# Optimization experiments

Hardware: AMD Instinct MI355X
Metric: run time of the kernel (lower is better)

Reference implementation:

```python
import jax, jax.numpy as jnp
import numpy as np

# Dims derived from module build() with d_model=256
D_MODEL = 256
EXPAND = 2
D_STATE = 16
K_CONV = 4
CHUNK = 64
HEADDIM = 64
D_INNER = EXPAND * D_MODEL            # 512
NHEADS = D_INNER // HEADDIM           # 8
CONV_DIM = D_INNER + 2 * D_STATE      # 544
D_IN_PROJ = 3 * D_INNER + 2 * D_STATE + NHEADS  # 1576
BATCH, SEQ = 4, 4096


def setup_inputs() -> dict:
    key = jax.random.key(0)
    ks = jax.random.split(key, 11)
    def rn(k, shape, s=1.0):
        return jax.random.normal(k, shape, dtype=jnp.float32) * s
    return {
        "x": rn(ks[0], (BATCH, SEQ, D_MODEL)),
        "W_in": rn(ks[1], (D_MODEL, D_IN_PROJ), D_MODEL ** -0.5),
        "conv_w": rn(ks[2], (K_CONV, CONV_DIM), 0.3),
        "conv_b": rn(ks[3], (CONV_DIM,), 0.1),
        "A_log": rn(ks[4], (NHEADS, 2), 0.5),
        "dt_bias": rn(ks[5], (NHEADS,), 0.1),
        "D": rn(ks[6], (2 * NHEADS, 1), 0.5),
        "init_conv_state": rn(ks[7], (1, K_CONV, CONV_DIM), 0.1),
        "init_ssm_state": rn(ks[8], (1, 1, NHEADS, HEADDIM, D_STATE, 2), 0.1),
        "norm_w": rn(ks[9], (2 * D_INNER,), 0.5),
        "W_out": rn(ks[10], (2 * D_INNER, D_MODEL), (2 * D_INNER) ** -0.5),
    }


def _exp_segsum(a):
    # a: (..., T) complex. Returns exp(segsum(a)): lower-triangular (incl. diag)
    # with entry [i,j] = exp(sum_{j<d<=i} a_d), zero strictly above the diagonal.
    T = a.shape[-1]
    cs = jnp.cumsum(a, axis=-1)
    seg = cs[..., :, None] - cs[..., None, :]
    mask = jnp.tril(jnp.ones((T, T), dtype=bool))
    seg = jnp.where(mask, seg, 0.0)  # keep exp finite / grad-safe off-band
    return jnp.where(mask, jnp.exp(seg), 0.0)


def reference(x, W_in, conv_w, conv_b, A_log, dt_bias, D, init_conv_state,
              init_ssm_state, norm_w, W_out):
    b, L, _ = x.shape
    zxbcdt = x @ W_in  # (b, L, 3*d_inner + 2*d_state + nheads)
    z = zxbcdt[..., : 2 * D_INNER]
    xBC = zxbcdt[..., 2 * D_INNER: 3 * D_INNER + 2 * D_STATE]
    dt_raw = zxbcdt[..., 3 * D_INNER + 2 * D_STATE:]
    # dt scalar in call is 1/30, then *30 -> net factor 1
    dt = jnp.clip(jnp.exp(dt_raw + dt_bias), 0.0, 6.0)  # (b, L, h)

    # causal depthwise conv1d with learned initial conv state, relu6 activation
    prefix = jnp.broadcast_to(init_conv_state, (b, K_CONV, CONV_DIM))
    full = jnp.concatenate([prefix, xBC], axis=1)  # (b, K_CONV + L, conv_dim)
    conv = conv_b + sum(conv_w[j] * full[:, 1 + j: 1 + j + L] for j in range(K_CONV))
    xBC = jnp.clip(conv, 0.0, 6.0)  # relu6, last L of the L+1 valid outputs

    xin = xBC[..., :D_INNER]
    Bm = xBC[..., D_INNER: D_INNER + D_STATE].astype(jnp.complex64)
    Cm = xBC[..., D_INNER + D_STATE:].astype(jnp.complex64)
    xh = xin.reshape(b, L, NHEADS, HEADDIM).astype(jnp.complex64)

    A = -jnp.exp(A_log[:, 0]) + 1j * A_log[:, 1]  # (h,) complex
    dtc = dt.astype(jnp.complex64)
    Adt = A * dtc              # (b, L, h)
    xdt = xh * dtc[..., None]  # (b, L, h, p)

    # ---- chunked SSD (Mamba2-style) with complex state ----
    c = L // CHUNK
    xc = xdt.reshape(b, c, CHUNK, NHEADS, HEADDIM)
    Ac = Adt.reshape(b, c, CHUNK, NHEADS).transpose(0, 3, 1, 2)  # (b, h, c, l)
    Bc = Bm.reshape(b, c, CHUNK, D_STATE)
    Cc = Cm.reshape(b, c, CHUNK, D_STATE)

    A_cum = jnp.cumsum(Ac, axis=-1)          # (b, h, c, l)
    Lmat = _exp_segsum(Ac)                   # (b, h, c, l, l)
    Y_diag = jnp.einsum('bcln,bcsn,bhcls,bcshp->bclhp', Cc, Bc, Lmat, xc)

    decay_states = jnp.exp(A_cum[..., -1:] - A_cum)  # (b, h, c, l)
    states = jnp.einsum('bcln,bhcl,bclhp->bchpn', Bc, decay_states, xc)

    init_stat = init_ssm_state[:, 0, ..., 0] + 1j * init_ssm_state[:, 0, ..., 1]
    init_stat = jnp.broadcast_to(init_stat, (b, NHEADS, HEADDIM, D_STATE))[:, None]
    states = jnp.concatenate([init_stat, states], axis=1)  # (b, c+1, h, p, n)

    decay_chunk = _exp_segsum(jnp.pad(A_cum[..., -1], ((0, 0), (0, 0), (1, 0))))
    new_states = jnp.einsum('bhzc,bchpn->bzhpn', decay_chunk, states)
    Y_off = jnp.einsum('bcln,bchpn,bhcl->bclhp', Cc, new_states[:, :-1], jnp.exp(A_cum))

    Y = (Y_diag + Y_off).reshape(b, L, NHEADS, HEADDIM)  # complex

    # 'b l h p c -> b l (h c) p' : interleave real/imag per head
    y2 = jnp.stack([Y.real, Y.imag], axis=3).reshape(b, L, 2 * NHEADS, HEADDIM)
    xr = xin.reshape(b, L, NHEADS, HEADDIM)
    x2 = jnp.stack([xr, jnp.zeros_like(xr)], axis=3).reshape(b, L, 2 * NHEADS, HEADDIM)
    y2 = y2 + x2 * D  # D: (2h, 1) broadcasts over p
    y3 = y2.reshape(b, L, 2 * D_INNER)

    # RMSNorm gated by relu6(z)
    yz = y3 * jnp.clip(z, 0.0, 6.0)
    y4 = yz * jax.lax.rsqrt(jnp.mean(yz * yz, axis=-1, keepdims=True) + 1e-5) * norm_w
    return y4 @ W_out
```

## Files before the change

### kernel.cpp

```cpp
#include <hip/hip_runtime.h>
#include <math.h>

#define BATCHN 4
#define SEQL   4096
#define DMODEL 256
#define DIP    1576
#define DINNER 512
#define DZCOLS 1024
#define CONVD  544
#define NHEADS 8
#define HDIM   64
#define DSTATE 16
#define CHK    64
#define NCHUNK 64
#define MROWS  (BATCHN*SEQL)
#define NPAD   1664

typedef _Float16 half8 __attribute__((ext_vector_type(8)));
typedef _Float16 half4 __attribute__((ext_vector_type(4)));
typedef short    s16x8 __attribute__((ext_vector_type(8)));
typedef float    f32x4 __attribute__((ext_vector_type(4)));

__device__ __forceinline__ float clip6f(float x) { return fminf(fmaxf(x, 0.0f), 6.0f); }

__global__ __launch_bounds__(256) void k_cvt_x(const float* __restrict__ X,
                                               _Float16* __restrict__ A)
{
    const int gid = blockIdx.x * 256 + threadIdx.x;
    const float4 a = *reinterpret_cast<const float4*>(X + (size_t)gid * 8);
    const float4 b = *reinterpret_cast<const float4*>(X + (size_t)gid * 8 + 4);
    half8 h;
    h[0] = (_Float16)a.x; h[1] = (_Float16)a.y; h[2] = (_Float16)a.z; h[3] = (_Float16)a.w;
    h[4] = (_Float16)b.x; h[5] = (_Float16)b.y; h[6] = (_Float16)b.z; h[7] = (_Float16)b.w;
    *reinterpret_cast<half8*>(A + (size_t)gid * 8) = h;
}

__global__ __launch_bounds__(256) void k_cvt_win(const float* __restrict__ W,
                                                 _Float16* __restrict__ Bt)
{
    const int gid = blockIdx.x * 256 + threadIdx.x;
    const int k = gid & 255, n = gid >> 8;
    const float v = (n < DIP) ? W[(size_t)k * DIP + n] : 0.0f;
    Bt[gid] = (_Float16)v;
}

__global__ __launch_bounds__(256) void k_cvt_wout(const float* __restrict__ W,
                                                  const float* __restrict__ nw,
                                                  _Float16* __restrict__ Bt)
{
    const int gid = blockIdx.x * 256 + threadIdx.x;
    const int k = gid & 1023, n = gid >> 10;
    Bt[gid] = (_Float16)(W[(size_t)k * DMODEL + n] * nw[k]);
}

__global__ __launch_bounds__(256) void k_gemm_in(const _Float16* __restrict__ A,
                                                 const _Float16* __restrict__ Bt,
                                                 _Float16* __restrict__ zx,
                                                 float* __restrict__ dtraw)
{
    __shared__ _Float16 As[128 * 64];
    __shared__ _Float16 Bs[128 * 64];
    const int t  = threadIdx.x;
    const int orig = blockIdx.x;
    const int nid  = (orig & 7) * (13 * (MROWS / 128) / 8) + (orig >> 3);
    const int m0 = (nid / 13) * 128;
    const int n0 = (nid % 13) * 128;
    const int lane = t & 63, wid = t >> 6;
    const int wr = wid >> 1, wc = wid & 1;
    const int fr = lane & 15, fq = lane >> 4;
    const int lrow = lane >> 3;
    const int lch  = (lane & 7) ^ lrow;

    f32x4 acc[4][4];
#pragma unroll
    for (int m = 0; m < 4; ++m)
#pragma unroll
        for (int n = 0; n < 4; ++n)
#pragma unroll
            for (int e = 0; e < 4; ++e) acc[m][n][e] = 0.0f;

    for (int kt = 0; kt < DMODEL; kt += 64) {
#pragma unroll
        for (int q = 0; q < 4; ++q) {
            const int rbase = q * 32 + wid * 8;
            const size_t offA = (size_t)(m0 + rbase + lrow) * DMODEL + kt + lch * 8;
            const size_t offB = (size_t)(n0 + rbase + lrow) * DMODEL + kt + lch * 8;
            __builtin_amdgcn_global_load_lds(
                (const __attribute__((address_space(1))) void*)(A + offA),
                (__attribute__((address_space(3))) void*)(&As[rbase * 64]), 16, 0, 0);
            __builtin_amdgcn_global_load_lds(
                (const __attribute__((address_space(1))) void*)(Bt + offB),
                (__attribute__((address_space(3))) void*)(&Bs[rbase * 64]), 16, 0, 0);
        }
        __syncthreads();
#pragma unroll
        for (int ks = 0; ks < 64; ks += 32) {
            const int kc = (ks >> 3) + fq;
            half8 af[4], bf[4];
#pragma unroll
            for (int m = 0; m < 4; ++m) {
                const int R = wr * 64 + m * 16 + fr;
                af[m] = *reinterpret_cast<const half8*>(&As[R * 64 + ((kc ^ (R & 7)) << 3)]);
            }
#pragma unroll
            for (int n = 0; n < 4; ++n) {
                const int R = wc * 64 + n * 16 + fr;
                bf[n] = *reinterpret_cast<const half8*>(&Bs[R * 64 + ((kc ^ (R & 7)) << 3)]);
            }
#pragma unroll
            for (int m = 0; m < 4; ++m)
#pragma unroll
                for (int n = 0; n < 4; ++n)
                    acc[m][n] = __builtin_amdgcn_mfma_f32_16x16x32_f16(af[m], bf[n], acc[m][n], 0, 0, 0);
        }
        __syncthreads();
    }

#pragma unroll
    for (int m = 0; m < 4; ++m)
#pragma unroll
        for (int j = 0; j < 4; ++j) {
            const int row = m0 + wr * 64 + m * 16 + fq * 4 + j;
#pragma unroll
            for (int n = 0; n < 4; ++n) {
                const int col = n0 + wc * 64 + n * 16 + fr;
                const float v = acc[m][n][j];
                if (col < DIP) {
                    zx[(size_t)row * DIP + col] = (_Float16)v;
                    if (col >= 3 * DINNER + 2 * DSTATE)
                        dtraw[(size_t)row * 8 + (col - (3 * DINNER + 2 * DSTATE))] = v;
                }
            }
        }
}

__global__ __launch_bounds__(256) void k_conv(const _Float16* __restrict__ zx,
                                              const float* __restrict__ conv_w,
                                              const float* __restrict__ conv_b,
                                              const float* __restrict__ init_conv,
                                              _Float16* __restrict__ convout)
{
    const int NC8 = CONVD / 8;
    const int gid = blockIdx.x * 256 + threadIdx.x;
    if (gid >= MROWS * NC8) return;
    const int row  = gid / NC8;
    const int c    = (gid % NC8) * 8;
    const int b    = row / SEQL;
    const int tpos = row % SEQL;
    float acc[8];
    {
        const float4 b0 = *reinterpret_cast<const float4*>(conv_b + c);
        const float4 b1 = *reinterpret_cast<const float4*>(conv_b + c + 4);
        acc[0] = b0.x; acc[1] = b0.y; acc[2] = b0.z; acc[3] = b0.w;
        acc[4] = b1.x; acc[5] = b1.y; acc[6] = b1.z; acc[7] = b1.w;
    }
#pragma unroll
    for (int j = 0; j < 4; ++j) {
        const int srct = tpos - 3 + j;
        float v[8];
        if (srct >= 0) {
            const half8 hv = *reinterpret_cast<const half8*>(
                zx + (size_t)(b * SEQL + srct) * DIP + DZCOLS + c);
#pragma unroll
            for (int e = 0; e < 8; ++e) v[e] = (float)hv[e];
        } else {
            const float* ip = init_conv + (size_t)(tpos + 1 + j) * CONVD + c;
            const float4 i0 = *reinterpret_cast<const float4*>(ip);
            const float4 i1 = *reinterpret_cast<const float4*>(ip + 4);
            v[0] = i0.x; v[1] = i0.y; v[2] = i0.z; v[3] = i0.w;
            v[4] = i1.x; v[5] = i1.y; v[6] = i1.z; v[7] = i1.w;
        }
        const float* wp = conv_w + (size_t)j * CONVD + c;
        const float4 w0 = *reinterpret_cast<const float4*>(wp);
        const float4 w1 = *reinterpret_cast<const float4*>(wp + 4);
        const float w[8] = {w0.x, w0.y, w0.z, w0.w, w1.x, w1.y, w1.z, w1.w};
#pragma unroll
        for (int e = 0; e < 8; ++e) acc[e] = fmaf(w[e], v[e], acc[e]);
    }
    half8 hv;
#pragma unroll
    for (int e = 0; e < 8; ++e) hv[e] = (_Float16)clip6f(acc[e]);
    *reinterpret_cast<half8*>(convout + (size_t)row * CONVD + c) = hv;
}

__global__ __launch_bounds__(256) void k_states(const float* __restrict__ dtraw,
                                                const _Float16* __restrict__ conv,
                                                const float* __restrict__ A_log,
                                                const float* __restrict__ dt_bias,
                                                float* __restrict__ Acum,
                                                float* __restrict__ ctbuf,
                                                float* __restrict__ st)
{
    const int c = blockIdx.x, h = blockIdx.y, b = blockIdx.z;
    __shared__ float wr[CHK], wi[CHK];
    __shared__ float xs[CHK][HDIM];
    __shared__ float Bsh[CHK][DSTATE];
    const int t = threadIdx.x;

#pragma unroll
    for (int q = 0; q < 2; ++q) {
        const int g = t + q * 256;
        const int l = g >> 3, p8 = (g & 7) * 8;
        const half8 hv = *reinterpret_cast<const half8*>(
            conv + (size_t)(b * SEQL + c * CHK + l) * CONVD + h * HDIM + p8);
#pragma unroll
        for (int e = 0; e < 8; ++e) xs[l][p8 + e] = (float)hv[e];
    }
    if (t < 128) {
        const int l = t >> 1, n8 = (t & 1) * 8;
        const half8 hv = *reinterpret_cast<const half8*>(
            conv + (size_t)(b * SEQL + c * CHK + l) * CONVD + DINNER + n8);
#pragma unroll
        for (int e = 0; e < 8; ++e) Bsh[l][n8 + e] = (float)hv[e];
    }

    if (t < 64) {
        const int l = t;
        const int row = b * SEQL + c * CHK + l;
        const float dtv = fminf(__expf(dtraw[(size_t)row * 8 + h] + dt_bias[h]), 6.0f);
        const float Ar = -__expf(A_log[2 * h]);
        const float Ai = A_log[2 * h + 1];
        float cr = Ar * dtv, ci = Ai * dtv;
#pragma unroll
        for (int off = 1; off < 64; off <<= 1) {
            const float pr = __shfl_up(cr, off);
            const float pi = __shfl_up(ci, off);
            if (l >= off) { cr += pr; ci += pi; }
        }
        const size_t aidx = ((((size_t)b * NHEADS + h) * NCHUNK + c) * CHK + l) * 2;
        Acum[aidx] = cr; Acum[aidx + 1] = ci;
        const float ctr = __shfl(cr, 63), cti = __shfl(ci, 63);
        if (l == 63) {
            const size_t ci2 = (((size_t)b * NHEADS + h) * NCHUNK + c) * 2;
            ctbuf[ci2] = ctr; ctbuf[ci2 + 1] = cti;
        }
        const float e = __expf(ctr - cr);
        float sn, cn; sincosf(cti - ci, &sn, &cn);
        wr[l] = e * cn * dtv;
        wi[l] = e * sn * dtv;
    }
    __syncthreads();

    const int p = t >> 2, n0 = (t & 3) * 4;
    float accr[4] = {0.f, 0.f, 0.f, 0.f};
    float acci[4] = {0.f, 0.f, 0.f, 0.f};
    for (int l = 0; l < CHK; ++l) {
        const float xv = xs[l][p];
        const float xr = xv * wr[l];
        const float xi = xv * wi[l];
#pragma unroll
        for (int j = 0; j < 4; ++j) {
            const float bb = Bsh[l][n0 + j];
            accr[j] = fmaf(bb, xr, accr[j]);
            acci[j] = fmaf(bb, xi, acci[j]);
        }
    }
    const size_t sidx = (((((size_t)b * NCHUNK + c) * NHEADS + h) * HDIM + p) * DSTATE + n0) * 2;
    float4 o0 = make_float4(accr[0], acci[0], accr[1], acci[1]);
    float4 o1 = make_float4(accr[2], acci[2], accr[3], acci[3]);
    *reinterpret_cast<float4*>(st + sidx)     = o0;
    *reinterpret_cast<float4*>(st + sidx + 4) = o1;
}

__global__ __launch_bounds__(128) void k_scan(const float* __restrict__ ctbuf,
                                              const float* __restrict__ st,
                                              const float* __restrict__ init_ssm,
                                              float* __restrict__ Sin)
{
    const int pg = blockIdx.x;
    const int h = blockIdx.y, b = blockIdx.z;
    __shared__ float Tr[NCHUNK], Ti[NCHUNK];
    const int t = threadIdx.x;
    if (t < NCHUNK) {
        const size_t ci2 = (((size_t)b * NHEADS + h) * NCHUNK + t) * 2;
        const float e = __expf(ctbuf[ci2]);
        float sn, cn; sincosf(ctbuf[ci2 + 1], &sn, &cn);
        Tr[t] = e * cn; Ti[t] = e * sn;
    }
    __syncthreads();
    const int p = pg * 8 + (t >> 4), n = t & 15;
    const size_t ii = (((size_t)h * HDIM + p) * DSTATE + n) * 2;
    float Sr = init_ssm[ii], Si = init_ssm[ii + 1];
    for (int z = 0; z < NCHUNK; ++z) {
        const size_t idx = (((((size_t)b * NCHUNK + z) * NHEADS + h) * HDIM + p) * DSTATE + n) * 2;
        Sin[idx] = Sr; Sin[idx + 1] = Si;
        const float sr = st[idx], si = st[idx + 1];
        const float tr = Tr[z], ti = Ti[z];
        const float nr = fmaf(tr, Sr, fmaf(-ti, Si, sr));
        const float ni = fmaf(tr, Si, fmaf(ti, Sr, si));
        Sr = nr; Si = ni;
    }
}

__global__ __launch_bounds__(256) void k_yout(const _Float16* __restrict__ conv,
                                              const float* __restrict__ Acum,
                                              const float* __restrict__ Sin,
                                              const float* __restrict__ Dp,
                                              const float* __restrict__ dt_bias,
                                              const float* __restrict__ dtraw,
                                              const _Float16* __restrict__ zx,
                                              _Float16* __restrict__ A2)
{
    const int c = blockIdx.x, h = blockIdx.y, b = blockIdx.z;
    __shared__ _Float16 Csh[64][40];
    __shared__ _Float16 Bsh[64][40];
    __shared__ _Float16 Srs[64][40];
    __shared__ _Float16 Sis[64][40];
    __shared__ _Float16 Xt[64][72];
    __shared__ _Float16 Gr[64][72];
    __shared__ _Float16 Gi[64][72];
    __shared__ float dts[64], cumr[64], sl_[64], cl_[64], Er[64], Ei[64];
    const int t = threadIdx.x;
    const int lane = t & 63, w = t >> 6;
    const int fr = lane & 15, fq = lane >> 4;
    const int rowb = b * SEQL + c * CHK;

    if (t < 64) {
        const int l = t, row = rowb + l;
        dts[l] = fminf(__expf(dtraw[(size_t)row * 8 + h] + dt_bias[h]), 6.0f);
        const size_t aidx = ((((size_t)b * NHEADS + h) * NCHUNK + c) * CHK + l) * 2;
        const float cr = Acum[aidx], ci = Acum[aidx + 1];
        cumr[l] = cr;
        float sn, cn; sincosf(ci, &sn, &cn);
        sl_[l] = sn; cl_[l] = cn;
        const float e = __expf(cr);
        Er[l] = e * cn; Ei[l] = e * sn;
    }
    {
        const int l = t >> 2, n4 = (t & 3) * 4;
        const _Float16* cp = conv + (size_t)(rowb + l) * CONVD + DINNER;
        const half4 bv = *reinterpret_cast<const half4*>(cp + n4);
        const half4 cv = *reinterpret_cast<const half4*>(cp + DSTATE + n4);
        Bsh[l][n4 + 0] = bv[0]; Bsh[l][n4 + 1] = bv[1];
        Bsh[l][n4 + 2] = bv[2]; Bsh[l][n4 + 3] = bv[3];
        Csh[l][n4 + 0] = cv[0]; Csh[l][n4 + 1] = cv[1];
        Csh[l][n4 + 2] = cv[2]; Csh[l][n4 + 3] = cv[3];
        const float* sp = Sin + ((((size_t)b * NCHUNK + c) * NHEADS + h) * HDIM + l) * (DSTATE * 2) + n4 * 2;
        const float4 s0 = *reinterpret_cast<const float4*>(sp);
        const float4 s1 = *reinterpret_cast<const float4*>(sp + 4);
        Srs[l][n4 + 0] = (_Float16)s0.x; Sis[l][n4 + 0] = (_Float16)s0.y;
        Srs[l][n4 + 1] = (_Float16)s0.z; Sis[l][n4 + 1] = (_Float16)s0.w;
        Srs[l][n4 + 2] = (_Float16)s1.x; Sis[l][n4 + 2] = (_Float16)s1.y;
        Srs[l][n4 + 3] = (_Float16)s1.z; Sis[l][n4 + 3] = (_Float16)s1.w;
        const int z0 = 16 + (t & 3) * 4;
#pragma unroll
        for (int e = 0; e < 4; ++e) {
            Bsh[l][z0 + e] = (_Float16)0.0f;
            Csh[l][z0 + e] = (_Float16)0.0f;
            Srs[l][z0 + e] = (_Float16)0.0f;
            Sis[l][z0 + e] = (_Float16)0.0f;
        }
    }
    __syncthreads();

#pragma unroll
    for (int q = 0; q < 2; ++q) {
        const int g = t + q * 256;
        const int l = g >> 3, p8 = (g & 7) * 8;
        const half8 hv = *reinterpret_cast<const half8*>(
            conv + (size_t)(rowb + l) * CONVD + h * HDIM + p8);
        const float d = dts[l];
#pragma unroll
        for (int e = 0; e < 8; ++e)
            Xt[p8 + e][l] = (_Float16)((float)hv[e] * d);
    }

    const half8 afC = *reinterpret_cast<const half8*>(&Csh[w * 16 + fr][fq * 8]);
    f32x4 cb[4];
#pragma unroll
    for (int nf = 0; nf < 4; ++nf) {
        const half8 bfB = *reinterpret_cast<const half8*>(&Bsh[nf * 16 + fr][fq * 8]);
        f32x4 z = {0.f, 0.f, 0.f, 0.f};
        cb[nf] = __builtin_amdgcn_mfma_f32_16x16x32_f16(afC, bfB, z, 0, 0, 0);
    }
#pragma unroll
    for (int nf = 0; nf < 4; ++nf) {
        const int s = nf * 16 + fr;
        const float crs = cumr[s], sls = sl_[s], cls = cl_[s];
#pragma unroll
        for (int j = 0; j < 4; ++j) {
            const int l = w * 16 + fq * 4 + j;
            const float dr = fminf(cumr[l] - crs, 0.0f);
            const float e = __expf(dr);
            const float cd = cl_[l] * cls + sl_[l] * sls;
            const float sd = sl_[l] * cls - cl_[l] * sls;
            const float ge = (s <= l) ? cb[nf][j] * e : 0.0f;
            Gr[l][s] = (_Float16)(ge * cd);
            Gi[l][s] = (_Float16)(ge * sd);
        }
    }
    __syncthreads();

    f32x4 accr[4], acci[4];
#pragma unroll
    for (int nf = 0; nf < 4; ++nf)
#pragma unroll
        for (int e = 0; e < 4; ++e) { accr[nf][e] = 0.f; acci[nf][e] = 0.f; }
#pragma unroll
    for (int ks = 0; ks < 64; ks += 32) {
        const half8 ar = *reinterpret_cast<const half8*>(&Gr[w * 16 + fr][ks + fq * 8]);
        const half8 ai = *reinterpret_cast<const half8*>(&Gi[w * 16 + fr][ks + fq * 8]);
#pragma unroll
        for (int nf = 0; nf < 4; ++nf) {
            const half8 bx = *reinterpret_cast<const half8*>(&Xt[nf * 16 + fr][ks + fq * 8]);
            accr[nf] = __builtin_amdgcn_mfma_f32_16x16x32_f16(ar, bx, accr[nf], 0, 0, 0);
            acci[nf] = __builtin_amdgcn_mfma_f32_16x16x32_f16(ai, bx, acci[nf], 0, 0, 0);
        }
    }
    f32x4 orr[4], oii[4];
#pragma unroll
    for (int nf = 0; nf < 4; ++nf) {
        const half8 br = *reinterpret_cast<const half8*>(&Srs[nf * 16 + fr][fq * 8]);
        const half8 bi = *reinterpret_cast<const half8*>(&Sis[nf * 16 + fr][fq * 8]);
        f32x4 z = {0.f, 0.f, 0.f, 0.f};
        orr[nf] = __builtin_amdgcn_mfma_f32_16x16x32_f16(afC, br, z, 0, 0, 0);
        oii[nf] = __builtin_amdgcn_mfma_f32_16x16x32_f16(afC, bi, z, 0, 0, 0);
    }

    const float dcoef = Dp[2 * h];
#pragma unroll
    for (int nf = 0; nf < 4; ++nf) {
        const int p = nf * 16 + fr;
#pragma unroll
        for (int j = 0; j < 4; ++j) {
            const int l = w * 16 + fq * 4 + j;
            const int row = rowb + l;
            const float er = Er[l], ei = Ei[l];
            float yr = accr[nf][j] + er * orr[nf][j] - ei * oii[nf][j];
            float yi = acci[nf][j] + er * oii[nf][j] + ei * orr[nf][j];
            const float xinv = (float)conv[(size_t)row * CONVD + h * HDIM + p];
            yr = fmaf(xinv, dcoef, yr);
            const size_t zidx = (size_t)row * DIP + h * 128 + p;
            const float zr = (float)zx[zidx], zi2 = (float)zx[zidx + 64];
            const size_t aidx2 = (size_t)row * DZCOLS + h * 128 + p;
            A2[aidx2]      = (_Float16)(yr * clip6f(zr));
            A2[aidx2 + 64] = (_Float16)(yi * clip6f(zi2));
        }
    }
}

__global__ __launch_bounds__(256) void k_gemm_out(const _Float16* __restrict__ A,
                                                  const _Float16* __restrict__ Bt,
                                                  float* __restrict__ C)
{
    __shared__ _Float16 As[128][72];
    __shared__ _Float16 Bs[128][72];
    __shared__ float ssp[128][8];
    __shared__ float scl[128];
    const int t  = threadIdx.x;
    const int orig = blockIdx.x;
    const int nid  = (orig & 7) * 32 + (orig >> 3);
    const int m0 = (nid >> 1) * 128;
    const int n0 = (nid & 1) * 128;
    const int lane = t & 63, wid = t >> 6;
    const int wr = wid >> 1, wc = wid & 1;
    const int fr = lane & 15, fq = lane >> 4;

    f32x4 acc[4][4];
#pragma unroll
    for (int m = 0; m < 4; ++m)
#pragma unroll
        for (int n = 0; n < 4; ++n)
#pragma unroll
            for (int e = 0; e < 4; ++e) acc[m][n][e] = 0.0f;
    float ss[4] = {0.f, 0.f, 0.f, 0.f};

    for (int kt = 0; kt < DZCOLS; kt += 64) {
#pragma unroll
        for (int q = 0; q < 4; ++q) {
            const int idx = t + q * 256;
            const int r = idx >> 3, ch = idx & 7;
            const half8 av = *reinterpret_cast<const half8*>(
                A + (size_t)(m0 + r) * DZCOLS + kt + ch * 8);
            *reinterpret_cast<half8*>(&As[r][ch * 8]) = av;
            float s = 0.f;
#pragma unroll
            for (int e = 0; e < 8; ++e) { const float f = (float)av[e]; s = fmaf(f, f, s); }
            ss[q] += s;
            *reinterpret_cast<s16x8*>(&Bs[r][ch * 8]) =
                *reinterpret_cast<const s16x8*>(Bt + (size_t)(n0 + r) * DZCOLS + kt + ch * 8);
        }
        __syncthreads();
#pragma unroll
        for (int ks = 0; ks < 64; ks += 32) {
            half8 af[4], bf[4];
#pragma unroll
            for (int m = 0; m < 4; ++m)
                af[m] = *reinterpret_cast<const half8*>(&As[wr * 64 + m * 16 + fr][ks + fq * 8]);
#pragma unroll
            for (int n = 0; n < 4; ++n)
                bf[n] = *reinterpret_cast<const half8*>(&Bs[wc * 64 + n * 16 + fr][ks + fq * 8]);
#pragma unroll
            for (int m = 0; m < 4; ++m)
#pragma unroll
                for (int n = 0; n < 4; ++n)
                    acc[m][n] = __builtin_amdgcn_mfma_f32_16x16x32_f16(af[m], bf[n], acc[m][n], 0, 0, 0);
        }
        __syncthreads();
    }

#pragma unroll
    for (int q = 0; q < 4; ++q) ssp[(t >> 3) + q * 32][t & 7] = ss[q];
    __syncthreads();
    if (t < 128) {
        float s = 0.f;
#pragma unroll
        for (int ch = 0; ch < 8; ++ch) s += ssp[t][ch];
        scl[t] = rsqrtf(s * (1.0f / 1024.0f) + 1e-5f);
    }
    __syncthreads();

#pragma unroll
    for (int m = 0; m < 4; ++m)
#pragma unroll
        for (int j = 0; j < 4; ++j) {
            const int rloc = wr * 64 + m * 16 + fq * 4 + j;
            const int row = m0 + rloc;
            const float sc = scl[rloc];
#pragma unroll
            for (int n = 0; n < 4; ++n) {
                const int col = n0 + wc * 64 + n * 16 + fr;
                C[(size_t)row * DMODEL + col] = acc[m][n][j] * sc;
            }
        }
}

extern "C" void kernel_launch(void* const* d_in, const int* in_sizes, int n_in,
                              void* d_out, int out_size, void* d_ws, size_t ws_size,
                              hipStream_t stream)
{
    const float* x         = (const float*)d_in[0];
    const float* W_in      = (const float*)d_in[1];
    const float* conv_w    = (const float*)d_in[2];
    const float* conv_b    = (const float*)d_in[3];
    const float* A_log     = (const float*)d_in[4];
    const float* dt_bias   = (const float*)d_in[5];
    const float* Dp        = (const float*)d_in[6];
    const float* init_conv = (const float*)d_in[7];
    const float* init_ssm  = (const float*)d_in[8];
    const float* norm_w    = (const float*)d_in[9];
    const float* W_out     = (const float*)d_in[10];
    float* out = (float*)d_out;

    float* ws      = (float*)d_ws;
    float* dtraw   = ws;
    float* Acum    = dtraw + (size_t)MROWS * 8;
    float* ctbuf   = Acum + (size_t)BATCHN * NHEADS * NCHUNK * CHK * 2;
    float* stbuf   = ctbuf + (size_t)BATCHN * NHEADS * NCHUNK * 2;
    float* SinBuf  = stbuf + (size_t)BATCHN * NCHUNK * NHEADS * HDIM * DSTATE * 2;
    _Float16* zx      = (_Float16*)(SinBuf + (size_t)BATCHN * NCHUNK * NHEADS * HDIM * DSTATE * 2);
    _Float16* convout = zx + (size_t)MROWS * DIP;
    _Float16* A2      = convout + (size_t)MROWS * CONVD;
    _Float16* Bt16    = A2 + (size_t)MROWS * DZCOLS;
    _Float16* Wot     = Bt16 + (size_t)NPAD * DMODEL;
    _Float16* A16     = Wot + (size_t)DMODEL * DZCOLS;

    k_cvt_x<<<dim3(MROWS * DMODEL / 8 / 256), dim3(256), 0, stream>>>(x, A16);
    k_cvt_win<<<dim3(NPAD), dim3(256), 0, stream>>>(W_in, Bt16);
    k_cvt_wout<<<dim3(DZCOLS), dim3(256), 0, stream>>>(W_out, norm_w, Wot);

    k_gemm_in<<<dim3((NPAD / 128) * (MROWS / 128)), dim3(256), 0, stream>>>(
        A16, Bt16, zx, dtraw);

    const int convThreads = MROWS * (CONVD / 8);
    k_conv<<<(convThreads + 255) / 256, dim3(256), 0, stream>>>(
        zx, conv_w, conv_b, init_conv, convout);

    k_states<<<dim3(NCHUNK, NHEADS, BATCHN), dim3(256), 0, stream>>>(
        dtraw, convout, A_log, dt_bias, Acum, ctbuf, stbuf);

    k_scan<<<dim3(HDIM / 8, NHEADS, BATCHN), dim3(128), 0, stream>>>(
        ctbuf, stbuf, init_ssm, SinBuf);

    k_yout<<<dim3(NCHUNK, NHEADS, BATCHN), dim3(256), 0, stream>>>(
        convout, Acum, SinBuf, Dp, dt_bias, dtraw, zx, A2);

    k_gemm_out<<<dim3((DMODEL / 128) * (MROWS / 128)), dim3(256), 0, stream>>>(
        A2, Wot, out);
}
```

Baseline: 216.5 us.

## Enlarge input GEMM M-tile and stage epilogue through LDS for vector stores

The input projection GEMM now computes 256x128 tiles instead of 128x128. Each wave holds an 8x4 accumulator array, which halves the re-reads of the B tile. The epilogue stages fp16 results in reused shared memory, one 128-row half at a time, and writes zx with coalesced 16-byte stores in place of scattered 2-byte ones. The cost is more registers and LDS per block, extra barriers, and half as many blocks, which can hurt occupancy and load balance.

```diff
diff --git a/kernel.cpp b/kernel.cpp
--- a/kernel.cpp
+++ b/kernel.cpp
@@ -14,7 +14,6 @@
 #define CHK    64
 #define NCHUNK 64
 #define MROWS  (BATCHN*SEQL)
-#define NPAD   1664
 
 typedef _Float16 half8 __attribute__((ext_vector_type(8)));
 typedef _Float16 half4 __attribute__((ext_vector_type(4)));
@@ -58,12 +57,14 @@
                                                  _Float16* __restrict__ zx,
                                                  float* __restrict__ dtraw)
 {
-    __shared__ _Float16 As[128 * 64];
-    __shared__ _Float16 Bs[128 * 64];
+    __shared__ _Float16 lds[256 * 64 + 128 * 64];
+    _Float16* As = lds;
+    _Float16* Bs = lds + 256 * 64;
+    _Float16* Ost = lds;
     const int t  = threadIdx.x;
     const int orig = blockIdx.x;
-    const int nid  = (orig & 7) * (13 * (MROWS / 128) / 8) + (orig >> 3);
-    const int m0 = (nid / 13) * 128;
+    const int nid  = (orig & 7) * 104 + (orig >> 3);
+    const int m0 = (nid / 13) * 256;
     const int n0 = (nid % 13) * 128;
     const int lane = t & 63, wid = t >> 6;
     const int wr = wid >> 1, wc = wid & 1;
@@ -71,9 +72,9 @@
     const int lrow = lane >> 3;
     const int lch  = (lane & 7) ^ lrow;
 
-    f32x4 acc[4][4];
-#pragma unroll
-    for (int m = 0; m < 4; ++m)
+    f32x4 acc[8][4];
+#pragma unroll
+    for (int m = 0; m < 8; ++m)
 #pragma unroll
         for (int n = 0; n < 4; ++n)
 #pragma unroll
@@ -81,13 +82,17 @@
 
     for (int kt = 0; kt < DMODEL; kt += 64) {
 #pragma unroll
-        for (int q = 0; q < 4; ++q) {
+        for (int q = 0; q < 8; ++q) {
             const int rbase = q * 32 + wid * 8;
             const size_t offA = (size_t)(m0 + rbase + lrow) * DMODEL + kt + lch * 8;
-            const size_t offB = (size_t)(n0 + rbase + lrow) * DMODEL + kt + lch * 8;
             __builtin_amdgcn_global_load_lds(
                 (const __attribute__((address_space(1))) void*)(A + offA),
                 (__attribute__((address_space(3))) void*)(&As[rbase * 64]), 16, 0, 0);
+        }
+#pragma unroll
+        for (int q = 0; q < 4; ++q) {
+            const int rbase = q * 32 + wid * 8;
+            const size_t offB = (size_t)(n0 + rbase + lrow) * DMODEL + kt + lch * 8;
             __builtin_amdgcn_global_load_lds(
                 (const __attribute__((address_space(1))) void*)(Bt + offB),
                 (__attribute__((address_space(3))) void*)(&Bs[rbase * 64]), 16, 0, 0);
@@ -96,10 +101,10 @@
 #pragma unroll
         for (int ks = 0; ks < 64; ks += 32) {
             const int kc = (ks >> 3) + fq;
-            half8 af[4], bf[4];
-#pragma unroll
-            for (int m = 0; m < 4; ++m) {
-                const int R = wr * 64 + m * 16 + fr;
+            half8 af[8], bf[4];
+#pragma unroll
+            for (int m = 0; m < 8; ++m) {
+                const int R = wr * 128 + m * 16 + fr;
                 af[m] = *reinterpret_cast<const half8*>(&As[R * 64 + ((kc ^ (R & 7)) << 3)]);
             }
 #pragma unroll
@@ -108,7 +113,7 @@
                 bf[n] = *reinterpret_cast<const half8*>(&Bs[R * 64 + ((kc ^ (R & 7)) << 3)]);
             }
 #pragma unroll
-            for (int m = 0; m < 4; ++m)
+            for (int m = 0; m < 8; ++m)
 #pragma unroll
                 for (int n = 0; n < 4; ++n)
                     acc[m][n] = __builtin_amdgcn_mfma_f32_16x16x32_f16(af[m], bf[n], acc[m][n], 0, 0, 0);
@@ -117,21 +122,37 @@
     }
 
 #pragma unroll
-    for (int m = 0; m < 4; ++m)
-#pragma unroll
-        for (int j = 0; j < 4; ++j) {
-            const int row = m0 + wr * 64 + m * 16 + fq * 4 + j;
-#pragma unroll
-            for (int n = 0; n < 4; ++n) {
-                const int col = n0 + wc * 64 + n * 16 + fr;
-                const float v = acc[m][n][j];
-                if (col < DIP) {
-                    zx[(size_t)row * DIP + col] = (_Float16)v;
-                    if (col >= 3 * DINNER + 2 * DSTATE)
-                        dtraw[(size_t)row * 8 + (col - (3 * DINNER + 2 * DSTATE))] = v;
+    for (int h2 = 0; h2 < 2; ++h2) {
+        __syncthreads();
+        if (wr == h2) {
+#pragma unroll
+            for (int m = 0; m < 8; ++m)
+#pragma unroll
+                for (int j = 0; j < 4; ++j) {
+                    const int rl = m * 16 + fq * 4 + j;
+#pragma unroll
+                    for (int n = 0; n < 4; ++n) {
+                        const float v = acc[m][n][j];
+                        const int cl = wc * 64 + n * 16 + fr;
+                        Ost[rl * 136 + cl] = (_Float16)v;
+                        const int col = n0 + cl;
+                        if (col >= 3 * DINNER + 2 * DSTATE && col < DIP)
+                            dtraw[(size_t)(m0 + h2 * 128 + rl) * 8 +
+                                  (col - (3 * DINNER + 2 * DSTATE))] = v;
+                    }
                 }
-            }
-        }
+        }
+        __syncthreads();
+#pragma unroll
+        for (int v = 0; v < 8; ++v) {
+            const int idx = t + v * 256;
+            const int r = idx >> 4, c8 = (idx & 15) * 8;
+            const int col = n0 + c8;
+            if (col < DIP)
+                *reinterpret_cast<half8*>(zx + (size_t)(m0 + h2 * 128 + r) * DIP + col) =
+                    *reinterpret_cast<const half8*>(&Ost[r * 136 + c8]);
+        }
+    }
 }
 
 __global__ __launch_bounds__(256) void k_conv(const _Float16* __restrict__ zx,
@@ -552,14 +573,14 @@
     _Float16* convout = zx + (size_t)MROWS * DIP;
     _Float16* A2      = convout + (size_t)MROWS * CONVD;
     _Float16* Bt16    = A2 + (size_t)MROWS * DZCOLS;
-    _Float16* Wot     = Bt16 + (size_t)NPAD * DMODEL;
+    _Float16* Wot     = Bt16 + (size_t)1664 * DMODEL;
     _Float16* A16     = Wot + (size_t)DMODEL * DZCOLS;
 
     k_cvt_x<<<dim3(MROWS * DMODEL / 8 / 256), dim3(256), 0, stream>>>(x, A16);
-    k_cvt_win<<<dim3(NPAD), dim3(256), 0, stream>>>(W_in, Bt16);
+    k_cvt_win<<<dim3(1664), dim3(256), 0, stream>>>(W_in, Bt16);
     k_cvt_wout<<<dim3(DZCOLS), dim3(256), 0, stream>>>(W_out, norm_w, Wot);
 
-    k_gemm_in<<<dim3((NPAD / 128) * (MROWS / 128)), dim3(256), 0, stream>>>(
+    k_gemm_in<<<dim3((1664 / 128) * (MROWS / 256)), dim3(256), 0, stream>>>(
         A16, Bt16, zx, dtraw);
 
     const int convThreads = MROWS * (CONVD / 8);
```

After: 228.9 us. 5.8% more time.
